# Optimization experiments

Hardware: AMD Instinct MI355X
Metric: run time of the kernel (lower is better)

## Reference

```python
import jax, jax.numpy as jnp
import numpy as np

SIGMA = 1.0  # Gaussian perturbation scale


def setup_inputs() -> dict:
    key = jax.random.key(0)
    k1, k2, k3 = jax.random.split(key, 3)
    S, B, D = 64, 128, 10000
    theta = jax.random.normal(k1, (B, D), dtype=jnp.float32)
    y = jax.random.uniform(k2, (B, D), dtype=jnp.float32)
    noise = jax.random.normal(k3, (S, B, D), dtype=jnp.float32)  # eta = theta + SIGMA*noise
    return {"theta": theta, "y": y, "noise": noise}


def reference(theta, y, noise):
    # eta = ptb.sample(theta, samples=S): [S, B, D]
    eta = theta[None, :, :] + SIGMA * noise
    # oracle.call vectorized over (S, B): softmax over feature dim
    pi = jax.nn.softmax(eta, axis=-1)  # [S, B, D]
    # loss(pi[i], y) -> per-example vector [B]: MSE mean over features
    losses = jnp.mean((pi - y[None, :, :]) ** 2, axis=-1)  # [S, B]
    # val = losses.mean(dim=(0, 1)) -> scalar
    val = jnp.mean(losses)
    return val
```

## Files before the change

kernel.cpp:

```cpp
#include <hip/hip_runtime.h>

#define S_DIM 64
#define B_DIM 128
#define D_DIM 10000
#define NV4   2500
#define BLOCK 512
#define RPB   8
#define NBLK  (B_DIM * (S_DIM / RPB))
#define NROWS (S_DIM * B_DIM)
#define NWAVE (BLOCK / 64)
#define FULLIT 39

__global__ __launch_bounds__(BLOCK) void perturbed_loss_waverow(
    const float* __restrict__ theta,
    const float* __restrict__ y,
    const float* __restrict__ noise,
    float4* __restrict__ partials,
    float*  __restrict__ y2arr)
{
    __shared__ float Tlds[D_DIM];
    __shared__ float Vlds[D_DIM];
    __shared__ float redY[NWAVE];

    const int blk  = blockIdx.x;
    const int b    = blk >> 3;
    const int s0   = (blk & 7) * RPB;
    const int tid  = threadIdx.x;
    const int lane = tid & 63;
    const int wave = tid >> 6;

    const float4* th4 = reinterpret_cast<const float4*>(theta + (size_t)b * D_DIM);
    const float4* y4  = reinterpret_cast<const float4*>(y     + (size_t)b * D_DIM);
    float4* T4 = reinterpret_cast<float4*>(Tlds);
    float4* V4 = reinterpret_cast<float4*>(Vlds);

    float y2 = 0.0f;
    for (int i = tid; i < NV4; i += BLOCK) {
        float4 t  = th4[i];
        float4 yy = y4[i];
        float4 T, V;
        T.x = __expf(t.x); T.y = __expf(t.y);
        T.z = __expf(t.z); T.w = __expf(t.w);
        V.x = T.x * yy.x;  V.y = T.y * yy.y;
        V.z = T.z * yy.z;  V.w = T.w * yy.w;
        T4[i] = T;  V4[i] = V;
        y2 = fmaf(yy.x, yy.x, y2); y2 = fmaf(yy.y, yy.y, y2);
        y2 = fmaf(yy.z, yy.z, y2); y2 = fmaf(yy.w, yy.w, y2);
    }
    #pragma unroll
    for (int o = 32; o > 0; o >>= 1) y2 += __shfl_down(y2, o, 64);
    if (lane == 0) redY[wave] = y2;
    __syncthreads();
    if (tid == 0 && (blk & 7) == 0) {
        float t = 0.0f;
        #pragma unroll
        for (int w = 0; w < NWAVE; ++w) t += redY[w];
        y2arr[b] = t;
    }

    const int row = (s0 + wave) * B_DIM + b;
    const float4* nz4 = reinterpret_cast<const float4*>(noise + (size_t)row * D_DIM);

    float s = 0.0f, q = 0.0f, p = 0.0f;
    int i = lane;
    #pragma unroll 4
    for (int it = 0; it < FULLIT; ++it, i += 64) {
        float4 n = nz4[i];
        float4 T = T4[i];
        float4 V = V4[i];
        float e0 = __expf(n.x), e1 = __expf(n.y);
        float e2 = __expf(n.z), e3 = __expf(n.w);
        float t0 = T.x * e0, t1 = T.y * e1;
        float t2 = T.z * e2, t3 = T.w * e3;
        s += (t0 + t1) + (t2 + t3);
        q = fmaf(t0, t0, q); q = fmaf(t1, t1, q);
        q = fmaf(t2, t2, q); q = fmaf(t3, t3, q);
        p = fmaf(V.x, e0, p); p = fmaf(V.y, e1, p);
        p = fmaf(V.z, e2, p); p = fmaf(V.w, e3, p);
    }
    if (lane < 4) {
        const int it = FULLIT * 64 + lane;
        float4 n = nz4[it];
        float4 T = T4[it];
        float4 V = V4[it];
        float e0 = __expf(n.x), e1 = __expf(n.y);
        float e2 = __expf(n.z), e3 = __expf(n.w);
        float t0 = T.x * e0, t1 = T.y * e1;
        float t2 = T.z * e2, t3 = T.w * e3;
        s += (t0 + t1) + (t2 + t3);
        q = fmaf(t0, t0, q); q = fmaf(t1, t1, q);
        q = fmaf(t2, t2, q); q = fmaf(t3, t3, q);
        p = fmaf(V.x, e0, p); p = fmaf(V.y, e1, p);
        p = fmaf(V.z, e2, p); p = fmaf(V.w, e3, p);
    }
    #pragma unroll
    for (int o = 32; o > 0; o >>= 1) {
        s += __shfl_down(s, o, 64);
        q += __shfl_down(q, o, 64);
        p += __shfl_down(p, o, 64);
    }
    if (lane == 0) partials[row] = make_float4(s, q, p, 0.0f);
}

__global__ __launch_bounds__(256) void reduce_partials(
    const float4* __restrict__ partials,
    const float*  __restrict__ y2arr,
    float* __restrict__ out)
{
    __shared__ double red[4];
    const int tid  = threadIdx.x;
    const int lane = tid & 63;
    const int wave = tid >> 6;

    double acc = 0.0;
    for (int i = tid; i < NROWS; i += 256) {
        float4 r = partials[i];
        double invS = 1.0 / (double)r.x;
        acc += ((double)r.y * invS - 2.0 * (double)r.z) * invS
             + (double)y2arr[i & (B_DIM - 1)];
    }
    #pragma unroll
    for (int o = 32; o > 0; o >>= 1) acc += __shfl_down(acc, o, 64);
    if (lane == 0) red[wave] = acc;
    __syncthreads();
    if (tid == 0) {
        double t = ((red[0] + red[1]) + (red[2] + red[3]));
        out[0] = (float)(t / ((double)S_DIM * (double)B_DIM * (double)D_DIM));
    }
}

extern "C" void kernel_launch(void* const* d_in, const int* in_sizes, int n_in,
                              void* d_out, int out_size, void* d_ws, size_t ws_size,
                              hipStream_t stream) {
    const float* theta = (const float*)d_in[0];
    const float* y     = (const float*)d_in[1];
    const float* noise = (const float*)d_in[2];
    float* out       = (float*)d_out;
    float4* partials = (float4*)d_ws;
    float*  y2arr    = (float*)((char*)d_ws + NROWS * sizeof(float4));

    perturbed_loss_waverow<<<NBLK, BLOCK, 0, stream>>>(theta, y, noise,
                                                       partials, y2arr);
    reduce_partials<<<1, 256, 0, stream>>>(partials, y2arr, out);
}
```

Before: 80.92 us.

## Pack exp(theta) and exp(theta)*y as bf16 in LDS and reduce losses per block

Stores exp(theta) and exp(theta)*y as packed bf16 in one uint4 LDS array, halving shared memory per block from 80KB to 40KB so more blocks can be resident per CU. It adds a launch-bounds occupancy hint, lowers the unroll factor, and computes the per-row loss inside the main kernel so the final reduction reads 1024 doubles instead of 8192 float4s. The bf16 rounding of the softmax weights introduces relative error of about 0.4% per element, which may shift the scalar loss beyond tolerance.

After: 73.07 us. -9.7%, faster.

```diff
diff --git a/kernel.cpp b/kernel.cpp
--- a/kernel.cpp
+++ b/kernel.cpp
@@ -11,16 +11,30 @@
 #define NWAVE (BLOCK / 64)
 #define FULLIT 39
 
-__global__ __launch_bounds__(BLOCK) void perturbed_loss_waverow(
+static __device__ __forceinline__ unsigned bf16pack(float lo, float hi) {
+    unsigned a = __builtin_bit_cast(unsigned, lo);
+    unsigned b = __builtin_bit_cast(unsigned, hi);
+    a = (a + 0x7fffu + ((a >> 16) & 1u)) >> 16;
+    b = (b + 0x7fffu + ((b >> 16) & 1u)) & 0xffff0000u;
+    return (a & 0xffffu) | b;
+}
+static __device__ __forceinline__ float bf16lo(unsigned u) {
+    return __builtin_bit_cast(float, u << 16);
+}
+static __device__ __forceinline__ float bf16hi(unsigned u) {
+    return __builtin_bit_cast(float, u & 0xffff0000u);
+}
+
+__global__ __launch_bounds__(BLOCK, 8) void perturbed_loss_waverow(
     const float* __restrict__ theta,
     const float* __restrict__ y,
     const float* __restrict__ noise,
-    float4* __restrict__ partials,
+    double* __restrict__ blockloss,
     float*  __restrict__ y2arr)
 {
-    __shared__ float Tlds[D_DIM];
-    __shared__ float Vlds[D_DIM];
-    __shared__ float redY[NWAVE];
+    __shared__ uint4  TV[NV4];
+    __shared__ float  redY[NWAVE];
+    __shared__ double wloss[NWAVE];
 
     const int blk  = blockIdx.x;
     const int b    = blk >> 3;
@@ -31,19 +45,16 @@
 
     const float4* th4 = reinterpret_cast<const float4*>(theta + (size_t)b * D_DIM);
     const float4* y4  = reinterpret_cast<const float4*>(y     + (size_t)b * D_DIM);
-    float4* T4 = reinterpret_cast<float4*>(Tlds);
-    float4* V4 = reinterpret_cast<float4*>(Vlds);
 
     float y2 = 0.0f;
     for (int i = tid; i < NV4; i += BLOCK) {
         float4 t  = th4[i];
         float4 yy = y4[i];
-        float4 T, V;
-        T.x = __expf(t.x); T.y = __expf(t.y);
-        T.z = __expf(t.z); T.w = __expf(t.w);
-        V.x = T.x * yy.x;  V.y = T.y * yy.y;
-        V.z = T.z * yy.z;  V.w = T.w * yy.w;
-        T4[i] = T;  V4[i] = V;
+        unsigned tp0 = bf16pack(__expf(t.x), __expf(t.y));
+        unsigned tp1 = bf16pack(__expf(t.z), __expf(t.w));
+        unsigned wp0 = bf16pack(bf16lo(tp0) * yy.x, bf16hi(tp0) * yy.y);
+        unsigned wp1 = bf16pack(bf16lo(tp1) * yy.z, bf16hi(tp1) * yy.w);
+        TV[i] = make_uint4(tp0, tp1, wp0, wp1);
         y2 = fmaf(yy.x, yy.x, y2); y2 = fmaf(yy.y, yy.y, y2);
         y2 = fmaf(yy.z, yy.z, y2); y2 = fmaf(yy.w, yy.w, y2);
     }
@@ -63,35 +74,33 @@
 
     float s = 0.0f, q = 0.0f, p = 0.0f;
     int i = lane;
-    #pragma unroll 4
+    #pragma unroll 2
     for (int it = 0; it < FULLIT; ++it, i += 64) {
         float4 n = nz4[i];
-        float4 T = T4[i];
-        float4 V = V4[i];
+        uint4  u = TV[i];
         float e0 = __expf(n.x), e1 = __expf(n.y);
         float e2 = __expf(n.z), e3 = __expf(n.w);
-        float t0 = T.x * e0, t1 = T.y * e1;
-        float t2 = T.z * e2, t3 = T.w * e3;
+        float t0 = bf16lo(u.x) * e0, t1 = bf16hi(u.x) * e1;
+        float t2 = bf16lo(u.y) * e2, t3 = bf16hi(u.y) * e3;
         s += (t0 + t1) + (t2 + t3);
         q = fmaf(t0, t0, q); q = fmaf(t1, t1, q);
         q = fmaf(t2, t2, q); q = fmaf(t3, t3, q);
-        p = fmaf(V.x, e0, p); p = fmaf(V.y, e1, p);
-        p = fmaf(V.z, e2, p); p = fmaf(V.w, e3, p);
+        p = fmaf(bf16lo(u.z), e0, p); p = fmaf(bf16hi(u.z), e1, p);
+        p = fmaf(bf16lo(u.w), e2, p); p = fmaf(bf16hi(u.w), e3, p);
     }
     if (lane < 4) {
-        const int it = FULLIT * 64 + lane;
-        float4 n = nz4[it];
-        float4 T = T4[it];
-        float4 V = V4[it];
+        const int j = FULLIT * 64 + lane;
+        float4 n = nz4[j];
+        uint4  u = TV[j];
         float e0 = __expf(n.x), e1 = __expf(n.y);
         float e2 = __expf(n.z), e3 = __expf(n.w);
-        float t0 = T.x * e0, t1 = T.y * e1;
-        float t2 = T.z * e2, t3 = T.w * e3;
+        float t0 = bf16lo(u.x) * e0, t1 = bf16hi(u.x) * e1;
+        float t2 = bf16lo(u.y) * e2, t3 = bf16hi(u.y) * e3;
         s += (t0 + t1) + (t2 + t3);
         q = fmaf(t0, t0, q); q = fmaf(t1, t1, q);
         q = fmaf(t2, t2, q); q = fmaf(t3, t3, q);
-        p = fmaf(V.x, e0, p); p = fmaf(V.y, e1, p);
-        p = fmaf(V.z, e2, p); p = fmaf(V.w, e3, p);
+        p = fmaf(bf16lo(u.z), e0, p); p = fmaf(bf16hi(u.z), e1, p);
+        p = fmaf(bf16lo(u.w), e2, p); p = fmaf(bf16hi(u.w), e3, p);
     }
     #pragma unroll
     for (int o = 32; o > 0; o >>= 1) {
@@ -99,11 +108,21 @@
         q += __shfl_down(q, o, 64);
         p += __shfl_down(p, o, 64);
     }
-    if (lane == 0) partials[row] = make_float4(s, q, p, 0.0f);
+    if (lane == 0) {
+        double invS = 1.0 / (double)s;
+        wloss[wave] = ((double)q * invS - 2.0 * (double)p) * invS;
+    }
+    __syncthreads();
+    if (tid == 0) {
+        double t = 0.0;
+        #pragma unroll
+        for (int w = 0; w < NWAVE; ++w) t += wloss[w];
+        blockloss[blk] = t;
+    }
 }
 
-__global__ __launch_bounds__(256) void reduce_partials(
-    const float4* __restrict__ partials,
+__global__ __launch_bounds__(256) void reduce_final(
+    const double* __restrict__ blockloss,
     const float*  __restrict__ y2arr,
     float* __restrict__ out)
 {
@@ -113,12 +132,8 @@
     const int wave = tid >> 6;
 
     double acc = 0.0;
-    for (int i = tid; i < NROWS; i += 256) {
-        float4 r = partials[i];
-        double invS = 1.0 / (double)r.x;
-        acc += ((double)r.y * invS - 2.0 * (double)r.z) * invS
-             + (double)y2arr[i & (B_DIM - 1)];
-    }
+    for (int i = tid; i < NBLK; i += 256) acc += blockloss[i];
+    if (tid < B_DIM) acc += (double)S_DIM * (double)y2arr[tid];
     #pragma unroll
     for (int o = 32; o > 0; o >>= 1) acc += __shfl_down(acc, o, 64);
     if (lane == 0) red[wave] = acc;
@@ -135,11 +150,11 @@
     const float* theta = (const float*)d_in[0];
     const float* y     = (const float*)d_in[1];
     const float* noise = (const float*)d_in[2];
-    float* out       = (float*)d_out;
-    float4* partials = (float4*)d_ws;
-    float*  y2arr    = (float*)((char*)d_ws + NROWS * sizeof(float4));
+    float* out        = (float*)d_out;
+    double* blockloss = (double*)d_ws;
+    float*  y2arr     = (float*)((char*)d_ws + NBLK * sizeof(double));
 
     perturbed_loss_waverow<<<NBLK, BLOCK, 0, stream>>>(theta, y, noise,
-                                                       partials, y2arr);
-    reduce_partials<<<1, 256, 0, stream>>>(partials, y2arr, out);
+                                                       blockloss, y2arr);
+    reduce_final<<<1, 256, 0, stream>>>(blockloss, y2arr, out);
 }
```
